# Kernel tuning notes

Measured on AMD Instinct MI355X. Metric: run time of the kernel, lower is better.

The kernel has to match this reference:

```python
import jax, jax.numpy as jnp
import numpy as np

N_NODES = 100000
D_IN = 128
D_OUT = 128
N_EDGES = 1600000
BATCH = 500000
LN_EPS = 1e-5


def setup_inputs() -> dict:
    key = jax.random.key(0)
    ks = jax.random.split(key, 9)
    stdv = 1.0 / np.sqrt(D_OUT)
    return {
        "x": jax.random.randint(ks[0], (BATCH,), 0, N_NODES + 1, dtype=jnp.int64)
             if jax.config.jax_enable_x64 else jax.random.randint(ks[0], (BATCH,), 0, N_NODES + 1, dtype=jnp.int32),
        "embeddings": jax.random.normal(ks[1], (N_NODES, D_IN), dtype=jnp.float32),
        "weight": jax.random.uniform(ks[2], (D_IN, D_OUT), minval=-stdv, maxval=stdv, dtype=jnp.float32),
        "bias": jax.random.uniform(ks[3], (D_OUT,), minval=-stdv, maxval=stdv, dtype=jnp.float32),
        "vals": jax.random.uniform(ks[4], (N_EDGES,), dtype=jnp.float32),
        "rows": jax.random.randint(ks[5], (N_EDGES,), 0, N_NODES, dtype=jnp.int32),
        "cols": jax.random.randint(ks[6], (N_EDGES,), 0, N_NODES, dtype=jnp.int32),
        "gamma": jnp.ones((D_OUT,), dtype=jnp.float32),
        "beta": jnp.zeros((D_OUT,), dtype=jnp.float32),
    }


def reference(x, embeddings, weight, bias, vals, rows, cols, gamma, beta):
    n = embeddings.shape[0]
    # Conv_layer: dense linear + sparse adjacency matmul (SpMM via gather + segment_sum)
    h = embeddings @ weight + bias                       # [N, D_OUT]
    msg = vals[:, None] * h[cols]                        # [E, D_OUT]
    h = jax.ops.segment_sum(msg, rows, num_segments=n)   # [N, D_OUT]
    # relu then LayerNorm
    h = jax.nn.relu(h)
    mu = jnp.mean(h, axis=-1, keepdims=True)
    var = jnp.mean(jnp.square(h - mu), axis=-1, keepdims=True)
    h = (h - mu) * jax.lax.rsqrt(var + LN_EPS) * gamma + beta
    # masked gather into output table: valid indices are in [1, N]
    select = (x >= 1) & (x < n + 1)
    idx = jnp.clip(x - 1, 0, n - 1)
    final = jnp.where(select[:, None], h[idx, :], 0.0)   # [B, D_OUT]
    return final
```

## Files before the change

kernel.cpp:

```cpp
#include <hip/hip_runtime.h>
#include <hip/hip_bf16.h>

#define D 128

typedef __attribute__((ext_vector_type(8))) short s8v;
typedef __attribute__((ext_vector_type(4))) float f4v;

__device__ inline unsigned short bf16rne(float f) {
  unsigned u = __float_as_uint(f);
  u += 0x7fff + ((u >> 16) & 1);
  return (unsigned short)(u >> 16);
}
__device__ inline float bf2f(unsigned short h) {
  return __uint_as_float(((unsigned)h) << 16);
}

__global__ __launch_bounds__(256) void init_wt_cnt(
    const float* __restrict__ W, unsigned short* __restrict__ WT16,
    int* __restrict__ cnt, int n1) {
  const int b = blockIdx.x;
  if (b < 64) {
    int idx = b * 256 + threadIdx.x;
    int k = idx >> 7, n = idx & 127;
    WT16[n * 128 + k] = bf16rne(W[idx]);
  } else {
    int i = (b - 64) * 1024 + threadIdx.x * 4;
    if (i + 3 < n1) {
      *(int4*)(cnt + i) = make_int4(0, 0, 0, 0);
    } else {
      for (int j = i; j < n1; ++j) cnt[j] = 0;
    }
  }
}

__global__ __launch_bounds__(256) void gemm_hist(
    const float* __restrict__ emb, const unsigned short* __restrict__ WT16,
    const float* __restrict__ bias, unsigned short* __restrict__ A16,
    int nNodes, int gemmBlocks,
    const int* __restrict__ rows, int* __restrict__ cnt, int nEdges) {
  if ((int)blockIdx.x >= gemmBlocks) {
    int base = (((int)blockIdx.x - gemmBlocks) * 256 + threadIdx.x) * 4;
    if (base + 3 < nEdges) {
      int4 r = *(const int4*)(rows + base);
      atomicAdd(&cnt[r.x], 1);
      atomicAdd(&cnt[r.y], 1);
      atomicAdd(&cnt[r.z], 1);
      atomicAdd(&cnt[r.w], 1);
    } else {
      for (int e = base; e < nEdges; ++e) atomicAdd(&cnt[rows[e]], 1);
    }
    return;
  }
  const int tid = threadIdx.x;
  const int w = tid >> 6;
  const int lane = tid & 63;
  const int m = lane & 15;
  const int kb = lane >> 4;
  const int r0 = (int)blockIdx.x * 64 + w * 16;
  int rowA = r0 + m;
  if (rowA > nNodes - 1) rowA = nNodes - 1;
  const float* arow = emb + (size_t)rowA * D + kb * 8;

  f4v acc[8];
#pragma unroll
  for (int t = 0; t < 8; ++t) acc[t] = (f4v){0.f, 0.f, 0.f, 0.f};

#pragma unroll
  for (int ks = 0; ks < 4; ++ks) {
    const int k0 = ks * 32;
    float4 a0 = *(const float4*)(arow + k0);
    float4 a1 = *(const float4*)(arow + k0 + 4);
    s8v af;
    af[0] = (short)bf16rne(a0.x); af[1] = (short)bf16rne(a0.y);
    af[2] = (short)bf16rne(a0.z); af[3] = (short)bf16rne(a0.w);
    af[4] = (short)bf16rne(a1.x); af[5] = (short)bf16rne(a1.y);
    af[6] = (short)bf16rne(a1.z); af[7] = (short)bf16rne(a1.w);
#pragma unroll
    for (int nt = 0; nt < 8; ++nt) {
      int n = nt * 16 + m;
      s8v bf = *(const s8v*)&WT16[n * 128 + k0 + kb * 8];
      acc[nt] = __builtin_amdgcn_mfma_f32_16x16x32_bf16(af, bf, acc[nt], 0, 0, 0);
    }
  }

#pragma unroll
  for (int nt = 0; nt < 8; ++nt) {
    int col = nt * 16 + m;
    float bcol = bias[col];
#pragma unroll
    for (int reg = 0; reg < 4; ++reg) {
      int row = r0 + kb * 4 + reg;
      if (row < nNodes)
        A16[(size_t)row * D + col] = bf16rne(acc[nt][reg] + bcol);
    }
  }
}

__global__ __launch_bounds__(1024) void scan_local(
    const int* __restrict__ cnt, int* __restrict__ start,
    int* __restrict__ bsum, int n) {
  __shared__ int wsum[16];
  __shared__ int wpre[16];
  const int tid = threadIdx.x;
  const int lane = tid & 63;
  const int wid = tid >> 6;
  int i = blockIdx.x * 1024 + tid;
  int v = (i < n) ? cnt[i] : 0;
  int inc = v;
#pragma unroll
  for (int st = 1; st < 64; st <<= 1) {
    int t = __shfl_up(inc, st);
    if (lane >= st) inc += t;
  }
  if (lane == 63) wsum[wid] = inc;
  __syncthreads();
  if (tid < 16) {
    int wv = wsum[tid];
    int winc = wv;
#pragma unroll
    for (int st = 1; st < 16; st <<= 1) {
      int t = __shfl_up(winc, st);
      if (lane >= st) winc += t;
    }
    wpre[tid] = winc - wv;
    if (tid == 15) bsum[blockIdx.x] = winc;
  }
  __syncthreads();
  if (i < n) start[i] = inc - v + wpre[wid];
}

__global__ __launch_bounds__(1024) void scan_add(
    int* __restrict__ start, const int* __restrict__ bsum,
    int* __restrict__ cursor, int n, int nCur) {
  __shared__ int boff_s;
  const int tid = threadIdx.x;
  if (tid < 64) {
    int ssum = 0;
    for (int j = tid; j < (int)blockIdx.x; j += 64) ssum += bsum[j];
#pragma unroll
    for (int off = 32; off >= 1; off >>= 1) ssum += __shfl_xor(ssum, off);
    if (tid == 0) boff_s = ssum;
  }
  __syncthreads();
  const int boff = boff_s;
  int i = blockIdx.x * 1024 + tid;
  if (i < n) {
    int s = start[i] + boff;
    start[i] = s;
    if (i < nCur) cursor[i] = s;
  }
}

__global__ __launch_bounds__(256) void scatter_build(
    const int* __restrict__ rows, const int* __restrict__ cols,
    const float* __restrict__ vals, int* __restrict__ cursor,
    int2* __restrict__ edata, int nEdges) {
  int e = blockIdx.x * 256 + threadIdx.x;
  if (e >= nEdges) return;
  int r = rows[e];
  int p = atomicAdd(&cursor[r], 1);
  int2 cv;
  cv.x = cols[e];
  cv.y = __float_as_int(vals[e]);
  edata[p] = cv;
}

__global__ __launch_bounds__(256) void segsum_relu_ln(
    const unsigned short* __restrict__ A16, const int2* __restrict__ edata,
    const int* __restrict__ start, const float* __restrict__ gamma,
    const float* __restrict__ beta, unsigned short* __restrict__ H16, int nNodes) {
  int node = blockIdx.x * 4 + (threadIdx.x >> 6);
  if (node >= nNodes) return;
  const int lane = threadIdx.x & 63;
  const int g = lane >> 4;
  const int li = lane & 15;
  int p = start[node];
  const int pend = start[node + 1];

  float acc[8];
#pragma unroll
  for (int j = 0; j < 8; ++j) acc[j] = 0.f;

  for (; p < pend; p += 16) {
    int2 cv0 = make_int2(0, 0), cv1 = make_int2(0, 0);
    int2 cv2 = make_int2(0, 0), cv3 = make_int2(0, 0);
    int p0 = p + g, p1 = p + 4 + g, p2 = p + 8 + g, p3 = p + 12 + g;
    if (p0 < pend) cv0 = edata[p0];
    if (p1 < pend) cv1 = edata[p1];
    if (p2 < pend) cv2 = edata[p2];
    if (p3 < pend) cv3 = edata[p3];
    uint4 u0 = ((const uint4*)(A16 + (size_t)cv0.x * D))[li];
    uint4 u1 = ((const uint4*)(A16 + (size_t)cv1.x * D))[li];
    uint4 u2 = ((const uint4*)(A16 + (size_t)cv2.x * D))[li];
    uint4 u3 = ((const uint4*)(A16 + (size_t)cv3.x * D))[li];
    float v0 = __int_as_float(cv0.y);
    float v1 = __int_as_float(cv1.y);
    float v2 = __int_as_float(cv2.y);
    float v3 = __int_as_float(cv3.y);
    acc[0] += v0 * bf2f((unsigned short)(u0.x & 0xffff));
    acc[1] += v0 * bf2f((unsigned short)(u0.x >> 16));
    acc[2] += v0 * bf2f((unsigned short)(u0.y & 0xffff));
    acc[3] += v0 * bf2f((unsigned short)(u0.y >> 16));
    acc[4] += v0 * bf2f((unsigned short)(u0.z & 0xffff));
    acc[5] += v0 * bf2f((unsigned short)(u0.z >> 16));
    acc[6] += v0 * bf2f((unsigned short)(u0.w & 0xffff));
    acc[7] += v0 * bf2f((unsigned short)(u0.w >> 16));
    acc[0] += v1 * bf2f((unsigned short)(u1.x & 0xffff));
    acc[1] += v1 * bf2f((unsigned short)(u1.x >> 16));
    acc[2] += v1 * bf2f((unsigned short)(u1.y & 0xffff));
    acc[3] += v1 * bf2f((unsigned short)(u1.y >> 16));
    acc[4] += v1 * bf2f((unsigned short)(u1.z & 0xffff));
    acc[5] += v1 * bf2f((unsigned short)(u1.z >> 16));
    acc[6] += v1 * bf2f((unsigned short)(u1.w & 0xffff));
    acc[7] += v1 * bf2f((unsigned short)(u1.w >> 16));
    acc[0] += v2 * bf2f((unsigned short)(u2.x & 0xffff));
    acc[1] += v2 * bf2f((unsigned short)(u2.x >> 16));
    acc[2] += v2 * bf2f((unsigned short)(u2.y & 0xffff));
    acc[3] += v2 * bf2f((unsigned short)(u2.y >> 16));
    acc[4] += v2 * bf2f((unsigned short)(u2.z & 0xffff));
    acc[5] += v2 * bf2f((unsigned short)(u2.z >> 16));
    acc[6] += v2 * bf2f((unsigned short)(u2.w & 0xffff));
    acc[7] += v2 * bf2f((unsigned short)(u2.w >> 16));
    acc[0] += v3 * bf2f((unsigned short)(u3.x & 0xffff));
    acc[1] += v3 * bf2f((unsigned short)(u3.x >> 16));
    acc[2] += v3 * bf2f((unsigned short)(u3.y & 0xffff));
    acc[3] += v3 * bf2f((unsigned short)(u3.y >> 16));
    acc[4] += v3 * bf2f((unsigned short)(u3.z & 0xffff));
    acc[5] += v3 * bf2f((unsigned short)(u3.z >> 16));
    acc[6] += v3 * bf2f((unsigned short)(u3.w & 0xffff));
    acc[7] += v3 * bf2f((unsigned short)(u3.w >> 16));
  }
#pragma unroll
  for (int j = 0; j < 8; ++j) {
    acc[j] += __shfl_xor(acc[j], 16);
    acc[j] += __shfl_xor(acc[j], 32);
  }
  float s = 0.f, sq = 0.f;
#pragma unroll
  for (int j = 0; j < 8; ++j) {
    acc[j] = fmaxf(acc[j], 0.f);
    s += acc[j];
    sq += acc[j] * acc[j];
  }
#pragma unroll
  for (int off = 8; off >= 1; off >>= 1) {
    s += __shfl_xor(s, off);
    sq += __shfl_xor(sq, off);
  }
  float mean = s * (1.f / 128.f);
  float var = sq * (1.f / 128.f) - mean * mean;
  float rstd = rsqrtf(var + 1e-5f);

  float4 g0 = ((const float4*)gamma)[li * 2];
  float4 g1 = ((const float4*)gamma)[li * 2 + 1];
  float4 b0 = ((const float4*)beta)[li * 2];
  float4 b1 = ((const float4*)beta)[li * 2 + 1];
  if (g == 0) {
    unsigned o0 = bf16rne((acc[0] - mean) * rstd * g0.x + b0.x)
                | ((unsigned)bf16rne((acc[1] - mean) * rstd * g0.y + b0.y) << 16);
    unsigned o1 = bf16rne((acc[2] - mean) * rstd * g0.z + b0.z)
                | ((unsigned)bf16rne((acc[3] - mean) * rstd * g0.w + b0.w) << 16);
    unsigned o2 = bf16rne((acc[4] - mean) * rstd * g1.x + b1.x)
                | ((unsigned)bf16rne((acc[5] - mean) * rstd * g1.y + b1.y) << 16);
    unsigned o3 = bf16rne((acc[6] - mean) * rstd * g1.z + b1.z)
                | ((unsigned)bf16rne((acc[7] - mean) * rstd * g1.w + b1.w) << 16);
    uint4 o = make_uint4(o0, o1, o2, o3);
    ((uint4*)(H16 + (size_t)node * D))[li] = o;
  }
}

__global__ __launch_bounds__(256) void gather_out(
    const int* __restrict__ x, const unsigned short* __restrict__ H16,
    float* __restrict__ out, int batch, int nNodes) {
  long gid = (long)blockIdx.x * 256 + threadIdx.x;
  int b = (int)(gid >> 4);
  int j = (int)(gid & 15);
  if (b >= batch) return;
  int xv = x[b];
  f4v r0 = (f4v){0.f, 0.f, 0.f, 0.f};
  f4v r1 = (f4v){0.f, 0.f, 0.f, 0.f};
  if (xv >= 1 && xv <= nNodes) {
    uint4 u = ((const uint4*)(H16 + (size_t)(xv - 1) * D))[j];
    r0 = (f4v){bf2f((unsigned short)(u.x & 0xffff)), bf2f((unsigned short)(u.x >> 16)),
               bf2f((unsigned short)(u.y & 0xffff)), bf2f((unsigned short)(u.y >> 16))};
    r1 = (f4v){bf2f((unsigned short)(u.z & 0xffff)), bf2f((unsigned short)(u.z >> 16)),
               bf2f((unsigned short)(u.w & 0xffff)), bf2f((unsigned short)(u.w >> 16))};
  }
  f4v* o = (f4v*)out + gid * 2;
  __builtin_nontemporal_store(r0, o);
  __builtin_nontemporal_store(r1, o + 1);
}

extern "C" void kernel_launch(void* const* d_in, const int* in_sizes, int n_in,
                              void* d_out, int out_size, void* d_ws, size_t ws_size,
                              hipStream_t stream) {
  const int* x = (const int*)d_in[0];
  const float* emb = (const float*)d_in[1];
  const float* W = (const float*)d_in[2];
  const float* bias = (const float*)d_in[3];
  const float* vals = (const float*)d_in[4];
  const int* rows = (const int*)d_in[5];
  const int* cols = (const int*)d_in[6];
  const float* gamma = (const float*)d_in[7];
  const float* beta = (const float*)d_in[8];
  float* out = (float*)d_out;

  const int batch = in_sizes[0];
  const int nNodes = in_sizes[1] / D;
  const int nEdges = in_sizes[4];
  const int n1 = nNodes + 1;
  const int nb = (n1 + 1023) / 1024;

  const size_t tab16 = (((size_t)nNodes * D * 2 + 255) / 256) * 256;
  const size_t cntB = (((size_t)n1 * 4 + 255) / 256) * 256;
  const size_t curB = (((size_t)nNodes * 4 + 255) / 256) * 256;
  const size_t bsB = (((size_t)nb * 4 + 255) / 256) * 256;
  const size_t wtB = (size_t)128 * 128 * 2;

  uint8_t* p = (uint8_t*)d_ws;
  unsigned short* A16 = (unsigned short*)p; p += tab16;
  unsigned short* H16 = (unsigned short*)p; p += tab16;
  unsigned short* WT16 = (unsigned short*)p; p += wtB;
  int* cnt = (int*)p; p += cntB;
  int* start = (int*)p; p += cntB;
  int* cursor = (int*)p; p += curB;
  int* bsum = (int*)p; p += bsB;
  int2* edata = (int2*)p;

  const int gemmBlocks = (nNodes + 63) / 64;
  const int histBlocks = (nEdges + 1023) / 1024;
  const int initBlocks = 64 + (n1 + 1023) / 1024;

  init_wt_cnt<<<initBlocks, 256, 0, stream>>>(W, WT16, cnt, n1);
  gemm_hist<<<gemmBlocks + histBlocks, 256, 0, stream>>>(
      emb, WT16, bias, A16, nNodes, gemmBlocks, rows, cnt, nEdges);
  scan_local<<<nb, 1024, 0, stream>>>(cnt, start, bsum, n1);
  scan_add<<<nb, 1024, 0, stream>>>(start, bsum, cursor, n1, nNodes);
  scatter_build<<<(nEdges + 255) / 256, 256, 0, stream>>>(rows, cols, vals, cursor, edata, nEdges);
  segsum_relu_ln<<<(nNodes + 3) / 4, 256, 0, stream>>>(A16, edata, start, gamma, beta, H16, nNodes);
  long gthreads = (long)batch * 16;
  gather_out<<<(int)((gthreads + 255) / 256), 256, 0, stream>>>(x, H16, out, batch, nNodes);
}
```

Before: 599.2 us.

## Fuse scan, scatter, segment-sum and gather into one cooperative persistent kernel

Replaces the five launches after the GEMM/histogram (scan_local, scan_add, scatter_build, segsum_relu_ln, gather_out) with a single cooperative kernel. It walks through the same phases in grid-stride loops separated by grid-wide syncs, with the grid capped by the occupancy query. The goal is to remove per-launch overhead and inter-kernel gaps. In exchange, phases run with a fixed, smaller grid and pay grid-sync costs, which may reduce latency hiding in the gather-heavy segment-sum. The fallback segsum kernel is also simplified from a 16-edge to a 4-edge inner loop, but it only runs if the cooperative launch fails.

```diff
diff --git a/kernel.cpp b/kernel.cpp
--- a/kernel.cpp
+++ b/kernel.cpp
@@ -1,5 +1,8 @@
 #include <hip/hip_runtime.h>
 #include <hip/hip_bf16.h>
+#include <hip/hip_cooperative_groups.h>
+
+namespace cg = cooperative_groups;
 
 #define D 128
 
@@ -96,6 +99,218 @@
   }
 }
 
+__global__ __launch_bounds__(512, 4) void mono_coop(
+    const unsigned short* __restrict__ A16,
+    const int* __restrict__ rows, const int* __restrict__ cols,
+    const float* __restrict__ vals,
+    const int* __restrict__ cnt, int* __restrict__ start,
+    int* __restrict__ cursor, int* __restrict__ bsum, int2* __restrict__ edata,
+    const float* __restrict__ gamma, const float* __restrict__ beta,
+    unsigned short* __restrict__ H16,
+    const int* __restrict__ x, float* __restrict__ out,
+    int nNodes, int nEdges, int batch) {
+  cg::grid_group gg = cg::this_grid();
+  const int tid = threadIdx.x;
+  const int lane = tid & 63;
+  const int wid = tid >> 6;
+  const int G = gridDim.x;
+  const int n1 = nNodes + 1;
+  __shared__ int wsum[8];
+  __shared__ int wpre[8];
+
+  const int nChunks = (n1 + 511) >> 9;
+  for (int c = blockIdx.x; c < nChunks; c += G) {
+    int i = (c << 9) + tid;
+    int v = (i < n1) ? cnt[i] : 0;
+    int inc = v;
+#pragma unroll
+    for (int st = 1; st < 64; st <<= 1) {
+      int t = __shfl_up(inc, st);
+      if (lane >= st) inc += t;
+    }
+    if (lane == 63) wsum[wid] = inc;
+    __syncthreads();
+    if (tid < 8) {
+      int wv = wsum[tid];
+      int winc = wv;
+#pragma unroll
+      for (int st = 1; st < 8; st <<= 1) {
+        int t = __shfl_up(winc, st);
+        if (lane >= st) winc += t;
+      }
+      wpre[tid] = winc - wv;
+      if (tid == 7) bsum[c] = winc;
+    }
+    __syncthreads();
+    if (i < n1) start[i] = inc - v + wpre[wid];
+    __syncthreads();
+  }
+  gg.sync();
+
+  if (blockIdx.x == 0) {
+    int v = (tid < nChunks) ? bsum[tid] : 0;
+    int inc = v;
+#pragma unroll
+    for (int st = 1; st < 64; st <<= 1) {
+      int t = __shfl_up(inc, st);
+      if (lane >= st) inc += t;
+    }
+    if (lane == 63) wsum[wid] = inc;
+    __syncthreads();
+    if (tid < 8) {
+      int wv = wsum[tid];
+      int winc = wv;
+#pragma unroll
+      for (int st = 1; st < 8; st <<= 1) {
+        int t = __shfl_up(winc, st);
+        if (lane >= st) winc += t;
+      }
+      wpre[tid] = winc - wv;
+    }
+    __syncthreads();
+    if (tid < nChunks) bsum[tid] = inc - v + wpre[wid];
+  }
+  gg.sync();
+
+  for (int i = blockIdx.x * 512 + tid; i < n1; i += G * 512) {
+    int s = start[i] + bsum[i >> 9];
+    start[i] = s;
+    if (i < nNodes) cursor[i] = s;
+  }
+  gg.sync();
+
+  for (int e = blockIdx.x * 512 + tid; e < nEdges; e += G * 512) {
+    int r = rows[e];
+    int p = atomicAdd(&cursor[r], 1);
+    int2 cv;
+    cv.x = cols[e];
+    cv.y = __float_as_int(vals[e]);
+    edata[p] = cv;
+  }
+  gg.sync();
+
+  for (int base = blockIdx.x * 8; base < nNodes; base += G * 8) {
+    int node = base + wid;
+    if (node < nNodes) {
+      const int g = lane >> 4;
+      const int li = lane & 15;
+      int p = start[node];
+      const int pend = start[node + 1];
+
+      float acc[8];
+#pragma unroll
+      for (int j = 0; j < 8; ++j) acc[j] = 0.f;
+
+      for (; p < pend; p += 16) {
+        int2 cv0 = make_int2(0, 0), cv1 = make_int2(0, 0);
+        int2 cv2 = make_int2(0, 0), cv3 = make_int2(0, 0);
+        int p0 = p + g, p1 = p + 4 + g, p2 = p + 8 + g, p3 = p + 12 + g;
+        if (p0 < pend) cv0 = edata[p0];
+        if (p1 < pend) cv1 = edata[p1];
+        if (p2 < pend) cv2 = edata[p2];
+        if (p3 < pend) cv3 = edata[p3];
+        uint4 u0 = ((const uint4*)(A16 + (size_t)cv0.x * D))[li];
+        uint4 u1 = ((const uint4*)(A16 + (size_t)cv1.x * D))[li];
+        uint4 u2 = ((const uint4*)(A16 + (size_t)cv2.x * D))[li];
+        uint4 u3 = ((const uint4*)(A16 + (size_t)cv3.x * D))[li];
+        float v0 = __int_as_float(cv0.y);
+        float v1 = __int_as_float(cv1.y);
+        float v2 = __int_as_float(cv2.y);
+        float v3 = __int_as_float(cv3.y);
+        acc[0] += v0 * bf2f((unsigned short)(u0.x & 0xffff));
+        acc[1] += v0 * bf2f((unsigned short)(u0.x >> 16));
+        acc[2] += v0 * bf2f((unsigned short)(u0.y & 0xffff));
+        acc[3] += v0 * bf2f((unsigned short)(u0.y >> 16));
+        acc[4] += v0 * bf2f((unsigned short)(u0.z & 0xffff));
+        acc[5] += v0 * bf2f((unsigned short)(u0.z >> 16));
+        acc[6] += v0 * bf2f((unsigned short)(u0.w & 0xffff));
+        acc[7] += v0 * bf2f((unsigned short)(u0.w >> 16));
+        acc[0] += v1 * bf2f((unsigned short)(u1.x & 0xffff));
+        acc[1] += v1 * bf2f((unsigned short)(u1.x >> 16));
+        acc[2] += v1 * bf2f((unsigned short)(u1.y & 0xffff));
+        acc[3] += v1 * bf2f((unsigned short)(u1.y >> 16));
+        acc[4] += v1 * bf2f((unsigned short)(u1.z & 0xffff));
+        acc[5] += v1 * bf2f((unsigned short)(u1.z >> 16));
+        acc[6] += v1 * bf2f((unsigned short)(u1.w & 0xffff));
+        acc[7] += v1 * bf2f((unsigned short)(u1.w >> 16));
+        acc[0] += v2 * bf2f((unsigned short)(u2.x & 0xffff));
+        acc[1] += v2 * bf2f((unsigned short)(u2.x >> 16));
+        acc[2] += v2 * bf2f((unsigned short)(u2.y & 0xffff));
+        acc[3] += v2 * bf2f((unsigned short)(u2.y >> 16));
+        acc[4] += v2 * bf2f((unsigned short)(u2.z & 0xffff));
+        acc[5] += v2 * bf2f((unsigned short)(u2.z >> 16));
+        acc[6] += v2 * bf2f((unsigned short)(u2.w & 0xffff));
+        acc[7] += v2 * bf2f((unsigned short)(u2.w >> 16));
+        acc[0] += v3 * bf2f((unsigned short)(u3.x & 0xffff));
+        acc[1] += v3 * bf2f((unsigned short)(u3.x >> 16));
+        acc[2] += v3 * bf2f((unsigned short)(u3.y & 0xffff));
+        acc[3] += v3 * bf2f((unsigned short)(u3.y >> 16));
+        acc[4] += v3 * bf2f((unsigned short)(u3.z & 0xffff));
+        acc[5] += v3 * bf2f((unsigned short)(u3.z >> 16));
+        acc[6] += v3 * bf2f((unsigned short)(u3.w & 0xffff));
+        acc[7] += v3 * bf2f((unsigned short)(u3.w >> 16));
+      }
+#pragma unroll
+      for (int j = 0; j < 8; ++j) {
+        acc[j] += __shfl_xor(acc[j], 16);
+        acc[j] += __shfl_xor(acc[j], 32);
+      }
+      float s = 0.f, sq = 0.f;
+#pragma unroll
+      for (int j = 0; j < 8; ++j) {
+        acc[j] = fmaxf(acc[j], 0.f);
+        s += acc[j];
+        sq += acc[j] * acc[j];
+      }
+#pragma unroll
+      for (int off = 8; off >= 1; off >>= 1) {
+        s += __shfl_xor(s, off);
+        sq += __shfl_xor(sq, off);
+      }
+      float mean = s * (1.f / 128.f);
+      float var = sq * (1.f / 128.f) - mean * mean;
+      float rstd = rsqrtf(var + 1e-5f);
+
+      float4 g0 = ((const float4*)gamma)[li * 2];
+      float4 g1 = ((const float4*)gamma)[li * 2 + 1];
+      float4 b0 = ((const float4*)beta)[li * 2];
+      float4 b1 = ((const float4*)beta)[li * 2 + 1];
+      if (g == 0) {
+        unsigned o0 = bf16rne((acc[0] - mean) * rstd * g0.x + b0.x)
+                    | ((unsigned)bf16rne((acc[1] - mean) * rstd * g0.y + b0.y) << 16);
+        unsigned o1 = bf16rne((acc[2] - mean) * rstd * g0.z + b0.z)
+                    | ((unsigned)bf16rne((acc[3] - mean) * rstd * g0.w + b0.w) << 16);
+        unsigned o2 = bf16rne((acc[4] - mean) * rstd * g1.x + b1.x)
+                    | ((unsigned)bf16rne((acc[5] - mean) * rstd * g1.y + b1.y) << 16);
+        unsigned o3 = bf16rne((acc[6] - mean) * rstd * g1.z + b1.z)
+                    | ((unsigned)bf16rne((acc[7] - mean) * rstd * g1.w + b1.w) << 16);
+        uint4 o = make_uint4(o0, o1, o2, o3);
+        ((uint4*)(H16 + (size_t)node * D))[li] = o;
+      }
+    }
+  }
+  gg.sync();
+
+  const long gthreads = (long)batch * 16;
+  for (long gid = (long)blockIdx.x * 512 + tid; gid < gthreads; gid += (long)G * 512) {
+    int b = (int)(gid >> 4);
+    int j = (int)(gid & 15);
+    int xv = x[b];
+    f4v r0 = (f4v){0.f, 0.f, 0.f, 0.f};
+    f4v r1 = (f4v){0.f, 0.f, 0.f, 0.f};
+    if (xv >= 1 && xv <= nNodes) {
+      uint4 u = ((const uint4*)(H16 + (size_t)(xv - 1) * D))[j];
+      r0 = (f4v){bf2f((unsigned short)(u.x & 0xffff)), bf2f((unsigned short)(u.x >> 16)),
+                 bf2f((unsigned short)(u.y & 0xffff)), bf2f((unsigned short)(u.y >> 16))};
+      r1 = (f4v){bf2f((unsigned short)(u.z & 0xffff)), bf2f((unsigned short)(u.z >> 16)),
+                 bf2f((unsigned short)(u.w & 0xffff)), bf2f((unsigned short)(u.w >> 16))};
+    }
+    f4v* o = (f4v*)out + gid * 2;
+    __builtin_nontemporal_store(r0, o);
+    __builtin_nontemporal_store(r1, o + 1);
+  }
+}
+
 __global__ __launch_bounds__(1024) void scan_local(
     const int* __restrict__ cnt, int* __restrict__ start,
     int* __restrict__ bsum, int n) {
@@ -176,59 +391,23 @@
   const int li = lane & 15;
   int p = start[node];
   const int pend = start[node + 1];
-
   float acc[8];
 #pragma unroll
   for (int j = 0; j < 8; ++j) acc[j] = 0.f;
-
-  for (; p < pend; p += 16) {
-    int2 cv0 = make_int2(0, 0), cv1 = make_int2(0, 0);
-    int2 cv2 = make_int2(0, 0), cv3 = make_int2(0, 0);
-    int p0 = p + g, p1 = p + 4 + g, p2 = p + 8 + g, p3 = p + 12 + g;
-    if (p0 < pend) cv0 = edata[p0];
-    if (p1 < pend) cv1 = edata[p1];
-    if (p2 < pend) cv2 = edata[p2];
-    if (p3 < pend) cv3 = edata[p3];
-    uint4 u0 = ((const uint4*)(A16 + (size_t)cv0.x * D))[li];
-    uint4 u1 = ((const uint4*)(A16 + (size_t)cv1.x * D))[li];
-    uint4 u2 = ((const uint4*)(A16 + (size_t)cv2.x * D))[li];
-    uint4 u3 = ((const uint4*)(A16 + (size_t)cv3.x * D))[li];
-    float v0 = __int_as_float(cv0.y);
-    float v1 = __int_as_float(cv1.y);
-    float v2 = __int_as_float(cv2.y);
-    float v3 = __int_as_float(cv3.y);
-    acc[0] += v0 * bf2f((unsigned short)(u0.x & 0xffff));
-    acc[1] += v0 * bf2f((unsigned short)(u0.x >> 16));
-    acc[2] += v0 * bf2f((unsigned short)(u0.y & 0xffff));
-    acc[3] += v0 * bf2f((unsigned short)(u0.y >> 16));
-    acc[4] += v0 * bf2f((unsigned short)(u0.z & 0xffff));
-    acc[5] += v0 * bf2f((unsigned short)(u0.z >> 16));
-    acc[6] += v0 * bf2f((unsigned short)(u0.w & 0xffff));
-    acc[7] += v0 * bf2f((unsigned short)(u0.w >> 16));
-    acc[0] += v1 * bf2f((unsigned short)(u1.x & 0xffff));
-    acc[1] += v1 * bf2f((unsigned short)(u1.x >> 16));
-    acc[2] += v1 * bf2f((unsigned short)(u1.y & 0xffff));
-    acc[3] += v1 * bf2f((unsigned short)(u1.y >> 16));
-    acc[4] += v1 * bf2f((unsigned short)(u1.z & 0xffff));
-    acc[5] += v1 * bf2f((unsigned short)(u1.z >> 16));
-    acc[6] += v1 * bf2f((unsigned short)(u1.w & 0xffff));
-    acc[7] += v1 * bf2f((unsigned short)(u1.w >> 16));
-    acc[0] += v2 * bf2f((unsigned short)(u2.x & 0xffff));
-    acc[1] += v2 * bf2f((unsigned short)(u2.x >> 16));
-    acc[2] += v2 * bf2f((unsigned short)(u2.y & 0xffff));
-    acc[3] += v2 * bf2f((unsigned short)(u2.y >> 16));
-    acc[4] += v2 * bf2f((unsigned short)(u2.z & 0xffff));
-    acc[5] += v2 * bf2f((unsigned short)(u2.z >> 16));
-    acc[6] += v2 * bf2f((unsigned short)(u2.w & 0xffff));
-    acc[7] += v2 * bf2f((unsigned short)(u2.w >> 16));
-    acc[0] += v3 * bf2f((unsigned short)(u3.x & 0xffff));
-    acc[1] += v3 * bf2f((unsigned short)(u3.x >> 16));
-    acc[2] += v3 * bf2f((unsigned short)(u3.y & 0xffff));
-    acc[3] += v3 * bf2f((unsigned short)(u3.y >> 16));
-    acc[4] += v3 * bf2f((unsigned short)(u3.z & 0xffff));
-    acc[5] += v3 * bf2f((unsigned short)(u3.z >> 16));
-    acc[6] += v3 * bf2f((unsigned short)(u3.w & 0xffff));
-    acc[7] += v3 * bf2f((unsigned short)(u3.w >> 16));
+  for (; p < pend; p += 4) {
+    int pp = p + g;
+    int2 cv = make_int2(0, 0);
+    if (pp < pend) cv = edata[pp];
+    float v = __int_as_float(cv.y);
+    uint4 u = ((const uint4*)(A16 + (size_t)cv.x * D))[li];
+    acc[0] += v * bf2f((unsigned short)(u.x & 0xffff));
+    acc[1] += v * bf2f((unsigned short)(u.x >> 16));
+    acc[2] += v * bf2f((unsigned short)(u.y & 0xffff));
+    acc[3] += v * bf2f((unsigned short)(u.y >> 16));
+    acc[4] += v * bf2f((unsigned short)(u.z & 0xffff));
+    acc[5] += v * bf2f((unsigned short)(u.z >> 16));
+    acc[6] += v * bf2f((unsigned short)(u.w & 0xffff));
+    acc[7] += v * bf2f((unsigned short)(u.w >> 16));
   }
 #pragma unroll
   for (int j = 0; j < 8; ++j) {
@@ -250,7 +429,6 @@
   float mean = s * (1.f / 128.f);
   float var = sq * (1.f / 128.f) - mean * mean;
   float rstd = rsqrtf(var + 1e-5f);
-
   float4 g0 = ((const float4*)gamma)[li * 2];
   float4 g1 = ((const float4*)gamma)[li * 2 + 1];
   float4 b0 = ((const float4*)beta)[li * 2];
@@ -309,12 +487,13 @@
   const int nNodes = in_sizes[1] / D;
   const int nEdges = in_sizes[4];
   const int n1 = nNodes + 1;
-  const int nb = (n1 + 1023) / 1024;
+  const int nb1024 = (n1 + 1023) / 1024;
+  const int nb512 = (n1 + 511) / 512;
 
   const size_t tab16 = (((size_t)nNodes * D * 2 + 255) / 256) * 256;
   const size_t cntB = (((size_t)n1 * 4 + 255) / 256) * 256;
   const size_t curB = (((size_t)nNodes * 4 + 255) / 256) * 256;
-  const size_t bsB = (((size_t)nb * 4 + 255) / 256) * 256;
+  const size_t bsB = (((size_t)((nb512 > nb1024 ? nb512 : nb1024) + 1) * 4 + 255) / 256) * 256;
   const size_t wtB = (size_t)128 * 128 * 2;
 
   uint8_t* p = (uint8_t*)d_ws;
@@ -334,10 +513,30 @@
   init_wt_cnt<<<initBlocks, 256, 0, stream>>>(W, WT16, cnt, n1);
   gemm_hist<<<gemmBlocks + histBlocks, 256, 0, stream>>>(
       emb, WT16, bias, A16, nNodes, gemmBlocks, rows, cnt, nEdges);
-  scan_local<<<nb, 1024, 0, stream>>>(cnt, start, bsum, n1);
-  scan_add<<<nb, 1024, 0, stream>>>(start, bsum, cursor, n1, nNodes);
-  scatter_build<<<(nEdges + 255) / 256, 256, 0, stream>>>(rows, cols, vals, cursor, edata, nEdges);
-  segsum_relu_ln<<<(nNodes + 3) / 4, 256, 0, stream>>>(A16, edata, start, gamma, beta, H16, nNodes);
-  long gthreads = (long)batch * 16;
-  gather_out<<<(int)((gthreads + 255) / 256), 256, 0, stream>>>(x, H16, out, batch, nNodes);
-}
+
+  int maxB = 0;
+  hipError_t qerr = hipOccupancyMaxActiveBlocksPerMultiprocessor(
+      &maxB, (const void*)mono_coop, 512, 0);
+  int G = 512;
+  if (qerr == hipSuccess && maxB > 0) {
+    int cap = maxB * 256;
+    if (cap < G) G = cap;
+  }
+  int nNodes_ = nNodes, nEdges_ = nEdges, batch_ = batch;
+  void* args[] = {
+      (void*)&A16, (void*)&rows, (void*)&cols, (void*)&vals,
+      (void*)&cnt, (void*)&start, (void*)&cursor, (void*)&bsum, (void*)&edata,
+      (void*)&gamma, (void*)&beta, (void*)&H16,
+      (void*)&x, (void*)&out, (void*)&nNodes_, (void*)&nEdges_, (void*)&batch_};
+  hipError_t lerr = hipLaunchCooperativeKernel(
+      (const void*)mono_coop, dim3(G), dim3(512), args, 0, stream);
+
+  if (lerr != hipSuccess) {
+    scan_local<<<nb1024, 1024, 0, stream>>>(cnt, start, bsum, n1);
+    scan_add<<<nb1024, 1024, 0, stream>>>(start, bsum, cursor, n1, nNodes);
+    scatter_build<<<(nEdges + 255) / 256, 256, 0, stream>>>(rows, cols, vals, cursor, edata, nEdges);
+    segsum_relu_ln<<<(nNodes + 3) / 4, 256, 0, stream>>>(A16, edata, start, gamma, beta, H16, nNodes);
+    long gthreads = (long)batch * 16;
+    gather_out<<<(int)((gthreads + 255) / 256), 256, 0, stream>>>(x, H16, out, batch, nNodes);
+  }
+}
```

New measurement: 857.5 us. +43.1%, slower.
